# Kernel tuning notes

Hardware: AMD Instinct MI355X
Metric: run time of the kernel (lower is better)

## Reference

```python
import jax, jax.numpy as jnp
import numpy as np

N_NODES = 100_000
N_EDGES = 1_600_000
IN_DIM = 64
OUT_DIM = 64
EPS = 1e-5


def setup_inputs() -> dict:
    key = jax.random.key(0)
    k1, k2, k3, k4, k5, k6 = jax.random.split(key, 6)
    node = jax.random.normal(k1, (N_NODES, 3), dtype=jnp.float32)
    features = jax.random.normal(k2, (N_NODES, IN_DIM), dtype=jnp.float32)
    # src column covers every node so torch.unique(edges[:,0]) == arange(N_NODES)
    src = (jnp.arange(N_EDGES, dtype=jnp.int64) % N_NODES)
    dst = jax.random.randint(k3, (N_EDGES,), 0, N_NODES, dtype=jnp.int64)
    edges = jnp.stack([src, dst], axis=1)
    # torch.nn.Linear weight: [out_dim, in_dim+3], no bias
    W = jax.random.normal(k4, (OUT_DIM, IN_DIM + 3), dtype=jnp.float32) / np.sqrt(IN_DIM + 3)
    gamma = jnp.ones((OUT_DIM,), dtype=jnp.float32)
    beta = jnp.zeros((OUT_DIM,), dtype=jnp.float32)
    return {"node": node, "features": features, "W": W, "gamma": gamma,
            "beta": beta, "edges": edges}


def reference(node, features, W, gamma, beta, edges):
    src = edges[:, 0]
    dst = edges[:, 1]
    # gather + concat: [E, in_dim + 3]
    msg = jnp.concatenate([features[dst], node[dst] - node[src]], axis=1)
    # linear (no bias): [E, out_dim]
    h = msg @ W.T
    # BatchNorm1d (training mode: biased batch statistics over E rows)
    mean = jnp.mean(h, axis=0)
    var = jnp.mean(jnp.square(h - mean), axis=0)
    h = (h - mean) * jax.lax.rsqrt(var + EPS) * gamma + beta
    h = jax.nn.relu(h)
    # scatter_reduce amax with include_self=True on a zeros tensor:
    # per-destination max, including the initial 0 (relu output >= 0 anyway)
    n = node.shape[0]
    pooled = jnp.zeros((n, h.shape[1]), dtype=features.dtype).at[src].max(h)
    return pooled
```

## Files before the change

kernel.cpp:

```cpp
#include <hip/hip_runtime.h>

#define N_NODES 100000
#define N_EDGES 1600000
#define EPS 1e-5f
#define NG 12500
#define GWAVES 2048

typedef __bf16    bf16x8 __attribute__((ext_vector_type(8)));
typedef _Float16  f16x2  __attribute__((ext_vector_type(2)));
typedef _Float16  f16x4  __attribute__((ext_vector_type(4)));
typedef float     f32x4  __attribute__((ext_vector_type(4)));
typedef unsigned int u32;
typedef u32       u32x4  __attribute__((ext_vector_type(4)));

__device__ __forceinline__ u32 pkmax(u32 a, u32 b) {
  u32 d; asm("v_pk_max_f16 %0,%1,%2" : "=v"(d) : "v"(a), "v"(b)); return d;
}
__device__ __forceinline__ u32 pkmin(u32 a, u32 b) {
  u32 d; asm("v_pk_min_f16 %0,%1,%2" : "=v"(d) : "v"(a), "v"(b)); return d;
}
__device__ __forceinline__ float halves_sum(u32 v, float c) {
  f16x2 p = __builtin_bit_cast(f16x2, v);
#if __has_builtin(__builtin_amdgcn_fdot2)
  f16x2 one2 = {(_Float16)1.0f, (_Float16)1.0f};
  return __builtin_amdgcn_fdot2(p, one2, c, false);
#else
  return c + (float)p[0] + (float)p[1];
#endif
}
__device__ __forceinline__ float halves_sq(u32 v, float c) {
  f16x2 p = __builtin_bit_cast(f16x2, v);
#if __has_builtin(__builtin_amdgcn_fdot2)
  return __builtin_amdgcn_fdot2(p, p, c, false);
#else
  float a = (float)p[0], b = (float)p[1];
  return fmaf(a, a, fmaf(b, b, c));
#endif
}

__global__ __launch_bounds__(256) void gemm_kernel(
    const float* __restrict__ nodep, const float* __restrict__ feat,
    const float* __restrict__ W, unsigned short* __restrict__ g,
    float* __restrict__ accum) {
  if (blockIdx.x == 0 && threadIdx.x < 128) accum[threadIdx.x] = 0.f;

  const int lane = threadIdx.x & 63;
  const int wave = (int)((blockIdx.x * blockDim.x + threadIdx.x) >> 6);
  const int c    = lane & 15;
  const int quad = lane >> 4;
  if (wave >= N_NODES / 16) return;

  bf16x8 Bfrag[4][3];
#pragma unroll
  for (int t = 0; t < 4; ++t) {
    const float* wrow = W + (t * 16 + c) * 67;
#pragma unroll
    for (int s = 0; s < 3; ++s) {
#pragma unroll
      for (int j = 0; j < 8; ++j) {
        int k = s * 32 + quad * 8 + j;
        Bfrag[t][s][j] = (k < 67) ? (__bf16)wrow[k] : (__bf16)0.0f;
      }
    }
  }

  const int v = wave * 16 + c;
  const f32x4* f4 = (const f32x4*)(feat + (size_t)v * 64 + quad * 8);
  f32x4 fa = f4[0], fb = f4[1];
  const f32x4* f4b = (const f32x4*)(feat + (size_t)v * 64 + 32 + quad * 8);
  f32x4 fc = f4b[0], fd = f4b[1];
  bf16x8 A0, A1;
#pragma unroll
  for (int j = 0; j < 4; ++j) {
    A0[j] = (__bf16)fa[j]; A0[j + 4] = (__bf16)fb[j];
    A1[j] = (__bf16)fc[j]; A1[j + 4] = (__bf16)fd[j];
  }
  bf16x8 A2;
#pragma unroll
  for (int j = 0; j < 8; ++j) A2[j] = (__bf16)0.0f;
  if (quad == 0) {
    const float* np = nodep + (size_t)v * 3;
    A2[0] = (__bf16)np[0];
    A2[1] = (__bf16)np[1];
    A2[2] = (__bf16)np[2];
  }

#pragma unroll
  for (int t = 0; t < 4; ++t) {
    f32x4 acc = {0.f, 0.f, 0.f, 0.f};
    acc = __builtin_amdgcn_mfma_f32_16x16x32_bf16(A0, Bfrag[t][0], acc, 0, 0, 0);
    acc = __builtin_amdgcn_mfma_f32_16x16x32_bf16(A1, Bfrag[t][1], acc, 0, 0, 0);
    acc = __builtin_amdgcn_mfma_f32_16x16x32_bf16(A2, Bfrag[t][2], acc, 0, 0, 0);
    unsigned short* gp = g + (size_t)(wave * 16 + quad * 4) * 64 + t * 16 + c;
#pragma unroll
    for (int r = 0; r < 4; ++r)
      gp[r * 64] = __builtin_bit_cast(unsigned short, (_Float16)acc[r]);
  }
}

__global__ __launch_bounds__(256) void gather_kernel(
    const float* __restrict__ nodep, const int* __restrict__ edges,
    const _Float16* __restrict__ g, const float* __restrict__ W,
    _Float16* __restrict__ gmax, _Float16* __restrict__ gmin,
    float* __restrict__ accum) {
  const int lane = threadIdx.x & 63;
  const int wave = (int)((blockIdx.x * blockDim.x + threadIdx.x) >> 6);
  const int ch = lane & 7;
  const int s  = lane >> 3;

  float sh[8], sq[8], nxS[8], nyS[8], nzS[8];
#pragma unroll
  for (int j = 0; j < 8; ++j) {
    sh[j] = 0.f; sq[j] = 0.f; nxS[j] = 0.f; nyS[j] = 0.f; nzS[j] = 0.f;
  }
  float Lx = 0.f, Ly = 0.f, Lz = 0.f;
  float Mxx = 0.f, Myy = 0.f, Mzz = 0.f, Mxy = 0.f, Mxz = 0.f, Myz = 0.f;

  int idxA[16], idxB[16];
  u32x4 rA[16], rB[16];
  float cAx, cAy, cAz, cBx, cBy, cBz;

#define LOAD_IDX(dst, cx, cy, cz, gx)                                   \
  {                                                                     \
    if ((gx) < NG) {                                                    \
      const int* ep = edges + 16 * (gx) + 2 * s + 1;                    \
      _Pragma("unroll") for (int k = 0; k < 16; ++k)                    \
          dst[k] = ep[2 * k * N_NODES];                                 \
      const float* np = nodep + (size_t)(8 * (gx) + s) * 3;             \
      cx = np[0]; cy = np[1]; cz = np[2];                               \
    } else {                                                            \
      _Pragma("unroll") for (int k = 0; k < 16; ++k) dst[k] = 0;        \
      cx = 0.f; cy = 0.f; cz = 0.f;                                     \
    }                                                                   \
  }

#define GATHER(r, idx)                                                  \
  { _Pragma("unroll") for (int k = 0; k < 16; ++k)                      \
      r[k] = *(const u32x4*)(g + (size_t)idx[k] * 64 + ch * 8); }

  auto process = [&](int grp, const u32x4* r, float nx, float ny, float nz) {
    const int i = 8 * grp + s;
    Lx += nx; Ly += ny; Lz += nz;
    Mxx = fmaf(nx, nx, Mxx); Myy = fmaf(ny, ny, Myy); Mzz = fmaf(nz, nz, Mzz);
    Mxy = fmaf(nx, ny, Mxy); Mxz = fmaf(nx, nz, Mxz); Myz = fmaf(ny, nz, Myz);

    float Sn[8];
#pragma unroll
    for (int j = 0; j < 8; ++j) Sn[j] = 0.f;
    u32 mx[4], mn[4];
#pragma unroll
    for (int p = 0; p < 8; ++p) {
      const u32x4 va = r[2 * p], vb = r[2 * p + 1];
#pragma unroll
      for (int q = 0; q < 4; ++q) {
        u32 m  = pkmax(va[q], vb[q]);
        u32 n2 = pkmin(va[q], vb[q]);
        if (p == 0) { mx[q] = m; mn[q] = n2; }
        else        { mx[q] = pkmax(mx[q], m); mn[q] = pkmin(mn[q], n2); }
        u32 plo = __builtin_amdgcn_perm(va[q], vb[q], 0x01000504u);
        u32 phi = __builtin_amdgcn_perm(va[q], vb[q], 0x03020706u);
        Sn[2 * q]     = halves_sum(plo, Sn[2 * q]);
        Sn[2 * q + 1] = halves_sum(phi, Sn[2 * q + 1]);
        sq[2 * q]     = halves_sq(plo, sq[2 * q]);
        sq[2 * q + 1] = halves_sq(phi, sq[2 * q + 1]);
      }
    }
    u32x4 wm = {mx[0], mx[1], mx[2], mx[3]};
    *(u32x4*)(gmax + (size_t)i * 64 + ch * 8) = wm;
    u32x4 wn = {mn[0], mn[1], mn[2], mn[3]};
    *(u32x4*)(gmin + (size_t)i * 64 + ch * 8) = wn;
#pragma unroll
    for (int j = 0; j < 8; ++j) {
      sh[j]  += Sn[j];
      nxS[j] = fmaf(nx, Sn[j], nxS[j]);
      nyS[j] = fmaf(ny, Sn[j], nyS[j]);
      nzS[j] = fmaf(nz, Sn[j], nzS[j]);
    }
  };

  int gA = wave;
  LOAD_IDX(idxA, cAx, cAy, cAz, gA);
  GATHER(rA, idxA);
  int gB = gA + GWAVES;
  LOAD_IDX(idxB, cBx, cBy, cBz, gB);

  while (true) {
    GATHER(rB, idxB);
    int gA2 = gB + GWAVES;
    LOAD_IDX(idxA, cAx, cAy, cAz, gA2);
    float pAx = cAx, pAy = cAy, pAz = cAz;
    process(gA, rA, pAx, pAy, pAz);
    if (gB >= NG) break;
    GATHER(rA, idxA);
    int gB2 = gA2 + GWAVES;
    float qBx = cBx, qBy = cBy, qBz = cBz;
    LOAD_IDX(idxB, cBx, cBy, cBz, gB2);
    process(gB, rB, qBx, qBy, qBz);
    if (gA2 >= NG) break;
    gA = gA2; gB = gB2;
  }

#pragma unroll
  for (int step = 8; step < 64; step <<= 1) {
#pragma unroll
    for (int j = 0; j < 8; ++j) {
      sh[j]  += __shfl_xor(sh[j], step, 64);
      sq[j]  += __shfl_xor(sq[j], step, 64);
      nxS[j] += __shfl_xor(nxS[j], step, 64);
      nyS[j] += __shfl_xor(nyS[j], step, 64);
      nzS[j] += __shfl_xor(nzS[j], step, 64);
    }
    Lx  += __shfl_xor(Lx, step, 64);  Ly  += __shfl_xor(Ly, step, 64);
    Lz  += __shfl_xor(Lz, step, 64);
    Mxx += __shfl_xor(Mxx, step, 64); Myy += __shfl_xor(Myy, step, 64);
    Mzz += __shfl_xor(Mzz, step, 64); Mxy += __shfl_xor(Mxy, step, 64);
    Mxz += __shfl_xor(Mxz, step, 64); Myz += __shfl_xor(Myz, step, 64);
  }

  __shared__ float sred[4][128];
  const int w = (int)(threadIdx.x >> 6);
  if (lane < 8) {
#pragma unroll
    for (int j = 0; j < 8; ++j) {
      int col = ch * 8 + j;
      const float* wr = W + col * 67 + 64;
      float w0 = wr[0], w1 = wr[1], w2 = wr[2];
      float sumc = w0 * Lx + w1 * Ly + w2 * Lz;
      float cS   = w0 * nxS[j] + w1 * nyS[j] + w2 * nzS[j];
      float wMw  = w0 * w0 * Mxx + w1 * w1 * Myy + w2 * w2 * Mzz
                 + 2.f * (w0 * w1 * Mxy + w0 * w2 * Mxz + w1 * w2 * Myz);
      sred[w][col]      = sh[j] - 16.f * sumc;
      sred[w][64 + col] = sq[j] - 2.f * cS + 16.f * wMw;
    }
  }
  __syncthreads();
  const int t = threadIdx.x;
  if (t < 128)
    atomicAdd(accum + t, (sred[0][t] + sred[1][t]) + (sred[2][t] + sred[3][t]));
#undef LOAD_IDX
#undef GATHER
}

__global__ __launch_bounds__(256) void finalize_kernel(
    const _Float16* __restrict__ gmax, const _Float16* __restrict__ gmin,
    const float* __restrict__ accum, const float* __restrict__ gamma,
    const float* __restrict__ beta, const float* __restrict__ nodep,
    const float* __restrict__ W, float* __restrict__ out) {
  __shared__ __align__(16) float ssl[128];
  __shared__ float wnl[192];
  const int t = threadIdx.x;
  if (t < 64) {
    const float inv_ne = 1.0f / (float)N_EDGES;
    float mean = accum[t] * inv_ne;
    float var  = fmaxf(accum[64 + t] * inv_ne - mean * mean, 0.f);
    float sc   = gamma[t] * rsqrtf(var + EPS);
    ssl[t]      = sc;
    ssl[64 + t] = beta[t] - mean * sc;
    wnl[3 * t]     = W[t * 67 + 64];
    wnl[3 * t + 1] = W[t * 67 + 65];
    wnl[3 * t + 2] = W[t * 67 + 66];
  }
  __syncthreads();

  const int idx = (blockIdx.x * 256 + t) * 4;
  const int i = idx >> 6, d0 = idx & 63;
  const float nx = nodep[3 * i], ny = nodep[3 * i + 1], nz = nodep[3 * i + 2];
  f32x4 scv = *(const f32x4*)&ssl[d0];
  bool needmax = (scv[0] >= 0.f) | (scv[1] >= 0.f) | (scv[2] >= 0.f) | (scv[3] >= 0.f);
  bool needmin = (scv[0] < 0.f) | (scv[1] < 0.f) | (scv[2] < 0.f) | (scv[3] < 0.f);
  f16x4 gx = {}, gn = {};
  if (needmax) gx = *(const f16x4*)(gmax + idx);
  if (needmin) gn = *(const f16x4*)(gmin + idx);
  f32x4 o;
#pragma unroll
  for (int j = 0; j < 4; ++j) {
    int d = d0 + j;
    float sc = scv[j], shf = ssl[64 + d];
    float v = (sc >= 0.f) ? (float)gx[j] : (float)gn[j];
    float c = fmaf(wnl[3 * d + 2], nz, fmaf(wnl[3 * d + 1], ny, wnl[3 * d] * nx));
    o[j] = fmaxf(fmaf(v - c, sc, shf), 0.f);
  }
  *(f32x4*)(out + idx) = o;
}

extern "C" void kernel_launch(void* const* d_in, const int* in_sizes, int n_in,
                              void* d_out, int out_size, void* d_ws, size_t ws_size,
                              hipStream_t stream) {
  const float* nodep = (const float*)d_in[0];
  const float* feat  = (const float*)d_in[1];
  const float* W     = (const float*)d_in[2];
  const float* gamma = (const float*)d_in[3];
  const float* beta  = (const float*)d_in[4];
  const int*   edges = (const int*)d_in[5];

  char* ws = (char*)d_ws;
  unsigned short* g = (unsigned short*)ws;
  _Float16* gmax = (_Float16*)(ws + 12800000);
  _Float16* gmin = (_Float16*)(ws + 25600000);
  float* accum   = (float*)(ws + 38400000);
  float* out     = (float*)d_out;

  gemm_kernel<<<1563, 256, 0, stream>>>(nodep, feat, W, g, accum);
  gather_kernel<<<512, 256, 0, stream>>>(nodep, edges, (const _Float16*)g, W,
                                         gmax, gmin, accum);
  finalize_kernel<<<6250, 256, 0, stream>>>(gmax, gmin, accum, gamma, beta,
                                            nodep, W, out);
}
```

Before: 150.2 us.

## Replace persistent double-buffered gather loop with one group per wave

The gather kernel no longer runs a persistent grid of 2048 waves with a software-pipelined A/B double buffer. It now launches one wave per 8-node group (3125 blocks), each doing a single gather, reduce and write. To absorb the much larger number of per-block atomics on the BatchNorm statistics, the accumulator is split into 8 replicas indexed by block, and the finalize kernel sums them. This trades explicit prefetch overlap for hardware occupancy-based latency hiding, but adds per-wave shuffle reductions and block-level atomics for every group instead of once per persistent wave.

```diff
diff --git a/kernel.cpp b/kernel.cpp
--- a/kernel.cpp
+++ b/kernel.cpp
@@ -4,7 +4,6 @@
 #define N_EDGES 1600000
 #define EPS 1e-5f
 #define NG 12500
-#define GWAVES 2048
 
 typedef __bf16    bf16x8 __attribute__((ext_vector_type(8)));
 typedef _Float16  f16x2  __attribute__((ext_vector_type(2)));
@@ -42,7 +41,9 @@
     const float* __restrict__ nodep, const float* __restrict__ feat,
     const float* __restrict__ W, unsigned short* __restrict__ g,
     float* __restrict__ accum) {
-  if (blockIdx.x == 0 && threadIdx.x < 128) accum[threadIdx.x] = 0.f;
+  if (blockIdx.x == 0) {
+    for (int k = threadIdx.x; k < 1024; k += 256) accum[k] = 0.f;
+  }
 
   const int lane = threadIdx.x & 63;
   const int wave = (int)((blockIdx.x * blockDim.x + threadIdx.x) >> 6);
@@ -107,108 +108,64 @@
   const int wave = (int)((blockIdx.x * blockDim.x + threadIdx.x) >> 6);
   const int ch = lane & 7;
   const int s  = lane >> 3;
-
-  float sh[8], sq[8], nxS[8], nyS[8], nzS[8];
+  const int i  = wave * 8 + s;
+
+  int idx[16];
+  const int* ep = edges + 2 * i + 1;
+#pragma unroll
+  for (int k = 0; k < 16; ++k) idx[k] = ep[2 * k * N_NODES];
+
+  u32x4 r[16];
+#pragma unroll
+  for (int k = 0; k < 16; ++k)
+    r[k] = *(const u32x4*)(g + (size_t)idx[k] * 64 + ch * 8);
+
+  const float* np = nodep + (size_t)i * 3;
+  const float nx = np[0], ny = np[1], nz = np[2];
+
+  float Sn[8], sq[8];
+#pragma unroll
+  for (int j = 0; j < 8; ++j) { Sn[j] = 0.f; sq[j] = 0.f; }
+  u32 mx[4], mn[4];
+#pragma unroll
+  for (int p = 0; p < 8; ++p) {
+    const u32x4 va = r[2 * p], vb = r[2 * p + 1];
+#pragma unroll
+    for (int q = 0; q < 4; ++q) {
+      u32 m  = pkmax(va[q], vb[q]);
+      u32 n2 = pkmin(va[q], vb[q]);
+      if (p == 0) { mx[q] = m; mn[q] = n2; }
+      else        { mx[q] = pkmax(mx[q], m); mn[q] = pkmin(mn[q], n2); }
+      u32 plo = __builtin_amdgcn_perm(va[q], vb[q], 0x01000504u);
+      u32 phi = __builtin_amdgcn_perm(va[q], vb[q], 0x03020706u);
+      Sn[2 * q]     = halves_sum(plo, Sn[2 * q]);
+      Sn[2 * q + 1] = halves_sum(phi, Sn[2 * q + 1]);
+      sq[2 * q]     = halves_sq(plo, sq[2 * q]);
+      sq[2 * q + 1] = halves_sq(phi, sq[2 * q + 1]);
+    }
+  }
+  u32x4 wm = {mx[0], mx[1], mx[2], mx[3]};
+  *(u32x4*)(gmax + (size_t)i * 64 + ch * 8) = wm;
+  u32x4 wn = {mn[0], mn[1], mn[2], mn[3]};
+  *(u32x4*)(gmin + (size_t)i * 64 + ch * 8) = wn;
+
+  float px[8], py[8], pz[8];
 #pragma unroll
   for (int j = 0; j < 8; ++j) {
-    sh[j] = 0.f; sq[j] = 0.f; nxS[j] = 0.f; nyS[j] = 0.f; nzS[j] = 0.f;
-  }
-  float Lx = 0.f, Ly = 0.f, Lz = 0.f;
-  float Mxx = 0.f, Myy = 0.f, Mzz = 0.f, Mxy = 0.f, Mxz = 0.f, Myz = 0.f;
-
-  int idxA[16], idxB[16];
-  u32x4 rA[16], rB[16];
-  float cAx, cAy, cAz, cBx, cBy, cBz;
-
-#define LOAD_IDX(dst, cx, cy, cz, gx)                                   \
-  {                                                                     \
-    if ((gx) < NG) {                                                    \
-      const int* ep = edges + 16 * (gx) + 2 * s + 1;                    \
-      _Pragma("unroll") for (int k = 0; k < 16; ++k)                    \
-          dst[k] = ep[2 * k * N_NODES];                                 \
-      const float* np = nodep + (size_t)(8 * (gx) + s) * 3;             \
-      cx = np[0]; cy = np[1]; cz = np[2];                               \
-    } else {                                                            \
-      _Pragma("unroll") for (int k = 0; k < 16; ++k) dst[k] = 0;        \
-      cx = 0.f; cy = 0.f; cz = 0.f;                                     \
-    }                                                                   \
-  }
-
-#define GATHER(r, idx)                                                  \
-  { _Pragma("unroll") for (int k = 0; k < 16; ++k)                      \
-      r[k] = *(const u32x4*)(g + (size_t)idx[k] * 64 + ch * 8); }
-
-  auto process = [&](int grp, const u32x4* r, float nx, float ny, float nz) {
-    const int i = 8 * grp + s;
-    Lx += nx; Ly += ny; Lz += nz;
-    Mxx = fmaf(nx, nx, Mxx); Myy = fmaf(ny, ny, Myy); Mzz = fmaf(nz, nz, Mzz);
-    Mxy = fmaf(nx, ny, Mxy); Mxz = fmaf(nx, nz, Mxz); Myz = fmaf(ny, nz, Myz);
-
-    float Sn[8];
-#pragma unroll
-    for (int j = 0; j < 8; ++j) Sn[j] = 0.f;
-    u32 mx[4], mn[4];
-#pragma unroll
-    for (int p = 0; p < 8; ++p) {
-      const u32x4 va = r[2 * p], vb = r[2 * p + 1];
-#pragma unroll
-      for (int q = 0; q < 4; ++q) {
-        u32 m  = pkmax(va[q], vb[q]);
-        u32 n2 = pkmin(va[q], vb[q]);
-        if (p == 0) { mx[q] = m; mn[q] = n2; }
-        else        { mx[q] = pkmax(mx[q], m); mn[q] = pkmin(mn[q], n2); }
-        u32 plo = __builtin_amdgcn_perm(va[q], vb[q], 0x01000504u);
-        u32 phi = __builtin_amdgcn_perm(va[q], vb[q], 0x03020706u);
-        Sn[2 * q]     = halves_sum(plo, Sn[2 * q]);
-        Sn[2 * q + 1] = halves_sum(phi, Sn[2 * q + 1]);
-        sq[2 * q]     = halves_sq(plo, sq[2 * q]);
-        sq[2 * q + 1] = halves_sq(phi, sq[2 * q + 1]);
-      }
-    }
-    u32x4 wm = {mx[0], mx[1], mx[2], mx[3]};
-    *(u32x4*)(gmax + (size_t)i * 64 + ch * 8) = wm;
-    u32x4 wn = {mn[0], mn[1], mn[2], mn[3]};
-    *(u32x4*)(gmin + (size_t)i * 64 + ch * 8) = wn;
+    px[j] = nx * Sn[j]; py[j] = ny * Sn[j]; pz[j] = nz * Sn[j];
+  }
+  float Lx = nx, Ly = ny, Lz = nz;
+  float Mxx = nx * nx, Myy = ny * ny, Mzz = nz * nz;
+  float Mxy = nx * ny, Mxz = nx * nz, Myz = ny * nz;
+#pragma unroll
+  for (int step = 8; step < 64; step <<= 1) {
 #pragma unroll
     for (int j = 0; j < 8; ++j) {
-      sh[j]  += Sn[j];
-      nxS[j] = fmaf(nx, Sn[j], nxS[j]);
-      nyS[j] = fmaf(ny, Sn[j], nyS[j]);
-      nzS[j] = fmaf(nz, Sn[j], nzS[j]);
-    }
-  };
-
-  int gA = wave;
-  LOAD_IDX(idxA, cAx, cAy, cAz, gA);
-  GATHER(rA, idxA);
-  int gB = gA + GWAVES;
-  LOAD_IDX(idxB, cBx, cBy, cBz, gB);
-
-  while (true) {
-    GATHER(rB, idxB);
-    int gA2 = gB + GWAVES;
-    LOAD_IDX(idxA, cAx, cAy, cAz, gA2);
-    float pAx = cAx, pAy = cAy, pAz = cAz;
-    process(gA, rA, pAx, pAy, pAz);
-    if (gB >= NG) break;
-    GATHER(rA, idxA);
-    int gB2 = gA2 + GWAVES;
-    float qBx = cBx, qBy = cBy, qBz = cBz;
-    LOAD_IDX(idxB, cBx, cBy, cBz, gB2);
-    process(gB, rB, qBx, qBy, qBz);
-    if (gA2 >= NG) break;
-    gA = gA2; gB = gB2;
-  }
-
-#pragma unroll
-  for (int step = 8; step < 64; step <<= 1) {
-#pragma unroll
-    for (int j = 0; j < 8; ++j) {
-      sh[j]  += __shfl_xor(sh[j], step, 64);
-      sq[j]  += __shfl_xor(sq[j], step, 64);
-      nxS[j] += __shfl_xor(nxS[j], step, 64);
-      nyS[j] += __shfl_xor(nyS[j], step, 64);
-      nzS[j] += __shfl_xor(nzS[j], step, 64);
+      Sn[j] += __shfl_xor(Sn[j], step, 64);
+      sq[j] += __shfl_xor(sq[j], step, 64);
+      px[j] += __shfl_xor(px[j], step, 64);
+      py[j] += __shfl_xor(py[j], step, 64);
+      pz[j] += __shfl_xor(pz[j], step, 64);
     }
     Lx  += __shfl_xor(Lx, step, 64);  Ly  += __shfl_xor(Ly, step, 64);
     Lz  += __shfl_xor(Lz, step, 64);
@@ -226,19 +183,19 @@
       const float* wr = W + col * 67 + 64;
       float w0 = wr[0], w1 = wr[1], w2 = wr[2];
       float sumc = w0 * Lx + w1 * Ly + w2 * Lz;
-      float cS   = w0 * nxS[j] + w1 * nyS[j] + w2 * nzS[j];
+      float cS   = w0 * px[j] + w1 * py[j] + w2 * pz[j];
       float wMw  = w0 * w0 * Mxx + w1 * w1 * Myy + w2 * w2 * Mzz
                  + 2.f * (w0 * w1 * Mxy + w0 * w2 * Mxz + w1 * w2 * Myz);
-      sred[w][col]      = sh[j] - 16.f * sumc;
+      sred[w][col]      = Sn[j] - 16.f * sumc;
       sred[w][64 + col] = sq[j] - 2.f * cS + 16.f * wMw;
     }
   }
   __syncthreads();
   const int t = threadIdx.x;
-  if (t < 128)
-    atomicAdd(accum + t, (sred[0][t] + sred[1][t]) + (sred[2][t] + sred[3][t]));
-#undef LOAD_IDX
-#undef GATHER
+  if (t < 128) {
+    float v = (sred[0][t] + sred[1][t]) + (sred[2][t] + sred[3][t]);
+    atomicAdd(accum + 128 * (blockIdx.x & 7) + t, v);
+  }
 }
 
 __global__ __launch_bounds__(256) void finalize_kernel(
@@ -250,9 +207,15 @@
   __shared__ float wnl[192];
   const int t = threadIdx.x;
   if (t < 64) {
+    float a = 0.f, b = 0.f;
+#pragma unroll
+    for (int rp = 0; rp < 8; ++rp) {
+      a += accum[rp * 128 + t];
+      b += accum[rp * 128 + 64 + t];
+    }
     const float inv_ne = 1.0f / (float)N_EDGES;
-    float mean = accum[t] * inv_ne;
-    float var  = fmaxf(accum[64 + t] * inv_ne - mean * mean, 0.f);
+    float mean = a * inv_ne;
+    float var  = fmaxf(b * inv_ne - mean * mean, 0.f);
     float sc   = gamma[t] * rsqrtf(var + EPS);
     ssl[t]      = sc;
     ssl[64 + t] = beta[t] - mean * sc;
@@ -301,8 +264,8 @@
   float* out     = (float*)d_out;
 
   gemm_kernel<<<1563, 256, 0, stream>>>(nodep, feat, W, g, accum);
-  gather_kernel<<<512, 256, 0, stream>>>(nodep, edges, (const _Float16*)g, W,
-                                         gmax, gmin, accum);
+  gather_kernel<<<NG / 4, 256, 0, stream>>>(nodep, edges, (const _Float16*)g,
+                                            W, gmax, gmin, accum);
   finalize_kernel<<<6250, 256, 0, stream>>>(gmax, gmin, accum, gamma, beta,
                                             nodep, W, out);
 }
```

After: 146.7 us, median of 2. 2.4% less time.
